# Kernel optimization log

Measured on AMD Instinct MI355X. Metric: run time of the kernel, lower is better.

## Reference

```python
import math
import jax, jax.numpy as jnp
import numpy as np

B, T, D = 2, 2048, 2048
NH, HD = 16, 48           # query heads, head dim
LAT, NLH = 256, 8         # latent dim, latent (kv) heads
EPS = 1e-5


def setup_inputs() -> dict:
    key = jax.random.key(0)
    ks = jax.random.split(key, 7)
    x = jax.random.normal(ks[0], (B, T, D), dtype=jnp.float32)
    # causal mask [B, 1, T, T]
    mask = jnp.broadcast_to(jnp.tril(jnp.ones((T, T), dtype=bool))[None, None], (B, 1, T, T))
    s = lambda fan_in: 1.0 / math.sqrt(fan_in)
    Wq = jax.random.normal(ks[1], (D, NH * HD), dtype=jnp.float32) * s(D)
    Wkv = jax.random.normal(ks[2], (D, LAT), dtype=jnp.float32) * s(D)
    w_norm = jnp.ones((LAT,), dtype=jnp.float32)
    Wk = jax.random.normal(ks[3], (LAT, NLH * HD), dtype=jnp.float32) * s(LAT)
    Wv = jax.random.normal(ks[4], (LAT, NLH * HD), dtype=jnp.float32) * s(LAT)
    Wo = jax.random.normal(ks[5], (NH * HD, D), dtype=jnp.float32) * s(NH * HD)
    return {"x": x, "mask": mask, "Wq": Wq, "Wkv": Wkv, "w_norm": w_norm,
            "Wk": Wk, "Wv": Wv, "Wo": Wo}


def rms_norm(x, weight, eps=EPS):
    var = jnp.mean(x * x, axis=-1, keepdims=True)
    return x * jax.lax.rsqrt(var + eps) * weight


def reference(x, mask, Wq, Wkv, w_norm, Wk, Wv, Wo):
    b, t, _ = x.shape
    q = (x @ Wq).reshape(b, t, NH, HD)                      # [B,T,NH,HD]
    kv_latent = rms_norm(x @ Wkv, w_norm)                   # [B,T,LAT]
    k = (kv_latent @ Wk).reshape(b, t, NLH, HD)             # [B,T,NLH,HD]
    v = (kv_latent @ Wv).reshape(b, t, NLH, HD)
    rep = NH // NLH
    k = jnp.repeat(k, rep, axis=2)                          # [B,T,NH,HD]
    v = jnp.repeat(v, rep, axis=2)
    q = q.transpose(0, 2, 1, 3)                             # [B,NH,T,HD]
    k = k.transpose(0, 2, 1, 3)
    v = v.transpose(0, 2, 1, 3)
    scale = 1.0 / math.sqrt(HD)
    scores = jnp.einsum('bhqd,bhkd->bhqk', q, k) * scale    # [B,NH,T,T]
    scores = jnp.where(mask, scores, -1e9)
    attn = jax.nn.softmax(scores, axis=-1)
    out = jnp.einsum('bhqk,bhkd->bhqd', attn, v)            # [B,NH,T,HD]
    out = out.transpose(0, 2, 1, 3).reshape(b, t, NH * HD)
    return out @ Wo                                          # [B,T,D]
```

## Files before the change

kernel.cpp:

```cpp
#include <hip/hip_runtime.h>
#include <hip/hip_bf16.h>

typedef __hip_bfloat16 bf16;
typedef __attribute__((ext_vector_type(8))) short short8;
typedef __attribute__((ext_vector_type(4))) float f32x4;

#define Bq   2
#define Tq   2048
#define Dq   2048
#define NHq  16
#define HDq  48
#define LATq 256
#define NLHq 8
#define QN   (NHq * HDq)
#define KVN  (NLHq * HDq)

__device__ __forceinline__ unsigned short f2u(float x) {
    __hip_bfloat16 h = __float2bfloat16(x);
    return *reinterpret_cast<unsigned short*>(&h);
}
__device__ __forceinline__ float u2f(unsigned short u) {
    return __uint_as_float((unsigned)u << 16);
}
__device__ __forceinline__ unsigned pk2(float a, float b) {
    return (unsigned)f2u(a) | ((unsigned)f2u(b) << 16);
}

__global__ void __launch_bounds__(256)
cvt_x(const float* __restrict__ in, bf16* __restrict__ out) {
    const size_t i = ((size_t)blockIdx.x * 256 + threadIdx.x) * 8;
    const float4 a = *(const float4*)&in[i];
    const float4 b = *(const float4*)&in[i + 4];
    uint4 u;
    u.x = pk2(a.x, a.y); u.y = pk2(a.z, a.w);
    u.z = pk2(b.x, b.y); u.w = pk2(b.z, b.w);
    *(uint4*)&out[i] = u;
}

__global__ void __launch_bounds__(256)
tr_w(const float* __restrict__ W, bf16* __restrict__ WT, int K, int N) {
    __shared__ float ts[32][33];
    const int n0 = blockIdx.x * 32, k0 = blockIdx.y * 32;
    const int t = threadIdx.x;
    const int r = t >> 3, c4 = (t & 7) * 4;
    const float4 v = *(const float4*)&W[(size_t)(k0 + r) * N + n0 + c4];
    ts[r][c4] = v.x; ts[r][c4 + 1] = v.y; ts[r][c4 + 2] = v.z; ts[r][c4 + 3] = v.w;
    __syncthreads();
    const unsigned u0 = pk2(ts[c4][r], ts[c4 + 1][r]);
    const unsigned u1 = pk2(ts[c4 + 2][r], ts[c4 + 3][r]);
    *(uint2*)&WT[(size_t)(n0 + r) * K + k0 + c4] = make_uint2(u0, u1);
}

template<int MODE>
__global__ void __launch_bounds__(512)
gemm128(const bf16* __restrict__ A, const bf16* __restrict__ BT,
        void* __restrict__ C0v, void* __restrict__ C1v, int K) {
    __shared__ short As[2][128 * 40];
    __shared__ short Bs[2][64 * 40];
    const int t  = threadIdx.x;
    const int m0 = blockIdx.x * 128;
    const int n0 = blockIdx.y * 64;
    const int w  = t >> 6;
    const int wm = (w & 3) * 32;
    const int wn = (w >> 2) * 32;
    const int lr = t & 15;
    const int quad = (t >> 4) & 3;
    const int sr = t >> 2, sc = t & 3;

    f32x4 acc[2][2];
    #pragma unroll
    for (int mi = 0; mi < 2; ++mi)
        #pragma unroll
        for (int ni = 0; ni < 2; ++ni) acc[mi][ni] = (f32x4){0.f, 0.f, 0.f, 0.f};

    int aoff[2], boff[2];
    #pragma unroll
    for (int mi = 0; mi < 2; ++mi) aoff[mi] = (wm + mi * 16 + lr) * 40 + quad * 8;
    #pragma unroll
    for (int ni = 0; ni < 2; ++ni) boff[ni] = (wn + ni * 16 + lr) * 40 + quad * 8;

    uint4 pa0, pb0;
    auto glo = [&](int kt) {
        const int kb = kt * 32 + sc * 8;
        pa0 = *(const uint4*)&A[(size_t)(m0 + sr) * K + kb];
        if (t < 256) pb0 = *(const uint4*)&BT[(size_t)(n0 + sr) * K + kb];
    };
    auto lwrite = [&](int bb) {
        *(uint4*)&As[bb][sr * 40 + sc * 8] = pa0;
        if (t < 256) *(uint4*)&Bs[bb][sr * 40 + sc * 8] = pb0;
    };

    const int nk = K / 32;
    glo(0);
    lwrite(0);
    glo(1);
    __syncthreads();
    int cur = 0;

    for (int kt = 0; kt < nk; ++kt) {
        short8 af[2], bfr[2];
        #pragma unroll
        for (int mi = 0; mi < 2; ++mi) af[mi] = *(const short8*)&As[cur][aoff[mi]];
        #pragma unroll
        for (int ni = 0; ni < 2; ++ni) bfr[ni] = *(const short8*)&Bs[cur][boff[ni]];
        #pragma unroll
        for (int mi = 0; mi < 2; ++mi)
            #pragma unroll
            for (int ni = 0; ni < 2; ++ni)
                acc[mi][ni] = __builtin_amdgcn_mfma_f32_16x16x32_bf16(af[mi], bfr[ni], acc[mi][ni], 0, 0, 0);
        if (kt + 1 < nk) lwrite(cur ^ 1);
        if (kt + 2 < nk) glo(kt + 2);
        __syncthreads();
        cur ^= 1;
    }

    #pragma unroll
    for (int mi = 0; mi < 2; ++mi)
        #pragma unroll
        for (int ni = 0; ni < 2; ++ni) {
            const int col = n0 + wn + ni * 16 + lr;
            #pragma unroll
            for (int r = 0; r < 4; ++r) {
                const int row = m0 + wm + mi * 16 + quad * 4 + r;
                const float v = acc[mi][ni][r];
                if constexpr (MODE == 0) {
                    if (col < QN) ((bf16*)C0v)[(size_t)row * QN + col] = __float2bfloat16(v);
                    else ((float*)C1v)[(size_t)row * LATq + (col - QN)] = v;
                } else if constexpr (MODE == 1) {
                    if (col < KVN) ((bf16*)C0v)[(size_t)row * KVN + col] = __float2bfloat16(v);
                    else ((bf16*)C1v)[(size_t)row * KVN + (col - KVN)] = __float2bfloat16(v);
                } else {
                    ((float*)C0v)[(size_t)row * Dq + col] = v;
                }
            }
        }
}

__global__ void __launch_bounds__(256)
mla_kvrms(const float* __restrict__ xkv, const float* __restrict__ wn,
          bf16* __restrict__ lat) {
    const int t = threadIdx.x;
    const int row = blockIdx.x * 4 + (t >> 6);
    const int lane = t & 63;
    const float4 v = *(const float4*)&xkv[(size_t)row * LATq + lane * 4];
    float ss = v.x * v.x + v.y * v.y + v.z * v.z + v.w * v.w;
    ss += __shfl_xor(ss, 1);  ss += __shfl_xor(ss, 2);  ss += __shfl_xor(ss, 4);
    ss += __shfl_xor(ss, 8);  ss += __shfl_xor(ss, 16); ss += __shfl_xor(ss, 32);
    const float rr = rsqrtf(ss * (1.0f / LATq) + 1e-5f);
    const float4 g = *(const float4*)&wn[lane * 4];
    const unsigned w0 = pk2(v.x * rr * g.x, v.y * rr * g.y);
    const unsigned w1 = pk2(v.z * rr * g.z, v.w * rr * g.w);
    *(uint2*)&lat[(size_t)row * LATq + lane * 4] = make_uint2(w0, w1);
}

__global__ void __launch_bounds__(512)
mla_attn(const bf16* __restrict__ q, const bf16* __restrict__ kk,
         const bf16* __restrict__ vv, bf16* __restrict__ ao) {
    __shared__ __align__(16) short Ks[2][64 * 48];
    __shared__ __align__(16) short Vt[2][48 * 72];
    __shared__ __align__(16) short Ps[8][16 * 72];
    const int t    = threadIdx.x;
    const int g    = blockIdx.x;
    const int qy   = blockIdx.y;
    const int b    = blockIdx.z;
    const int qt0  = (qy < 16) ? (qy << 1) : (63 - (qy << 1));
    const int qt   = b ? (31 - qt0) : qt0;
    const int w    = t >> 6;
    const int lane = t & 63;
    const int lr   = t & 15;
    const int quad = (t >> 4) & 3;
    const int hh   = w & 1;
    const int rh   = w >> 1;
    const int h    = g * 2 + hh;
    const float scale = 0.14433756729740643f;
    const short8 z8 = {0, 0, 0, 0, 0, 0, 0, 0};

    const int qloc = rh * 16 + lr;
    const int qg   = qt * 64 + qloc;
    const bf16* qr = q + (size_t)(b * Tq + qg) * QN + h * HDq;
    short8 qf0 = *(const short8*)(qr + quad * 8);
    const short8 q1 = *(const short8*)(qr + 32 + (quad & 1) * 8);
    short8 qf1 = (quad < 2) ? q1 : z8;

    const bf16* kb = kk + (size_t)b * Tq * KVN + g * HDq;
    const bf16* vb = vv + (size_t)b * Tq * KVN + g * HDq;

    float m = -1e30f, l = 0.f;
    f32x4 acc[3];
    #pragma unroll
    for (int dm = 0; dm < 3; ++dm) acc[dm] = (f32x4){0.f, 0.f, 0.f, 0.f};

    short* Pw = &Ps[w][0];
    uint4 pre[3];

    auto issue = [&](int tl) {
        if (w >= 4) return;
        #pragma unroll
        for (int r = 0; r < 3; ++r) {
            if (w < 2) {
                const int idx = (w * 3 + r) * 64 + lane;
                const int row = idx / 6, ch = idx - row * 6;
                pre[r] = *(const uint4*)(kb + (size_t)(tl * 64 + row) * KVN + ch * 8);
            } else {
                const int idx = ((w - 2) * 3 + r) * 64 + lane;
                const int kp = idx & 31, hc = idx >> 5;
                const bf16* src = vb + (size_t)(tl * 64 + 2 * kp) * KVN + hc * 4;
                const uint2 a2 = *(const uint2*)src;
                const uint2 b2 = *(const uint2*)(src + KVN);
                pre[r].x = a2.x; pre[r].y = a2.y; pre[r].z = b2.x; pre[r].w = b2.y;
            }
        }
    };
    auto lwrite = [&](int bb) {
        if (w >= 4) return;
        #pragma unroll
        for (int r = 0; r < 3; ++r) {
            if (w < 2) {
                const int idx = (w * 3 + r) * 64 + lane;
                const int row = idx / 6, ch = idx - row * 6;
                *(uint4*)&Ks[bb][row * 48 + ch * 8] = pre[r];
            } else {
                const int idx = ((w - 2) * 3 + r) * 64 + lane;
                const int kp = idx & 31, hc = idx >> 5;
                const unsigned short* uu = (const unsigned short*)&pre[r];
                #pragma unroll
                for (int j = 0; j < 4; ++j)
                    *(unsigned*)&Vt[bb][(hc * 4 + j) * 72 + 2 * kp] =
                        (unsigned)uu[j] | ((unsigned)uu[4 + j] << 16);
            }
        }
    };

    issue(0);
    lwrite(0);
    __syncthreads();
    int cur = 0;

    for (int tl = 0; tl <= qt; ++tl) {
        const bool pref = (tl < qt);
        if (pref) issue(tl + 1);

        f32x4 sc[4];
        #pragma unroll
        for (int mt = 0; mt < 4; ++mt) {
            const short8 k0 = *(const short8*)&Ks[cur][(mt * 16 + lr) * 48 + quad * 8];
            const short8 k1v = *(const short8*)&Ks[cur][(mt * 16 + lr) * 48 + 32 + (quad & 1) * 8];
            const short8 k1 = (quad < 2) ? k1v : z8;
            f32x4 s = (f32x4){0.f, 0.f, 0.f, 0.f};
            s = __builtin_amdgcn_mfma_f32_16x16x32_bf16(k0, qf0, s, 0, 0, 0);
            s = __builtin_amdgcn_mfma_f32_16x16x32_bf16(k1, qf1, s, 0, 0, 0);
            sc[mt] = s;
        }
        if (tl == qt) {
            #pragma unroll
            for (int mt = 0; mt < 4; ++mt)
                #pragma unroll
                for (int r = 0; r < 4; ++r)
                    if (mt * 16 + quad * 4 + r > qloc) sc[mt][r] = -1e30f;
        }
        float mx = -1e30f;
        #pragma unroll
        for (int mt = 0; mt < 4; ++mt)
            #pragma unroll
            for (int r = 0; r < 4; ++r) mx = fmaxf(mx, sc[mt][r]);
        mx = fmaxf(mx, __shfl_xor(mx, 16));
        mx = fmaxf(mx, __shfl_xor(mx, 32));
        const float mn = fmaxf(m, mx * scale);
        const float f  = __expf(m - mn);
        m = mn;
        float rs = 0.f;
        #pragma unroll
        for (int mt = 0; mt < 4; ++mt)
            #pragma unroll
            for (int r = 0; r < 4; ++r) {
                const float p = u2f(f2u(__expf(fmaf(sc[mt][r], scale, -mn))));
                sc[mt][r] = p;
                rs += p;
            }
        rs += __shfl_xor(rs, 16);
        rs += __shfl_xor(rs, 32);
        l = l * f + rs;
        #pragma unroll
        for (int dm = 0; dm < 3; ++dm)
            #pragma unroll
            for (int r = 0; r < 4; ++r) acc[dm][r] *= f;
        #pragma unroll
        for (int mt = 0; mt < 4; ++mt) {
            unsigned* pw = (unsigned*)&Pw[lr * 72 + mt * 16 + quad * 4];
            pw[0] = pk2(sc[mt][0], sc[mt][1]);
            pw[1] = pk2(sc[mt][2], sc[mt][3]);
        }
        const short8 pf0 = *(const short8*)&Pw[lr * 72 + quad * 8];
        const short8 pf1 = *(const short8*)&Pw[lr * 72 + 32 + quad * 8];
        #pragma unroll
        for (int dm = 0; dm < 3; ++dm) {
            const short8 v0 = *(const short8*)&Vt[cur][(dm * 16 + lr) * 72 + quad * 8];
            const short8 v1 = *(const short8*)&Vt[cur][(dm * 16 + lr) * 72 + 32 + quad * 8];
            acc[dm] = __builtin_amdgcn_mfma_f32_16x16x32_bf16(v0, pf0, acc[dm], 0, 0, 0);
            acc[dm] = __builtin_amdgcn_mfma_f32_16x16x32_bf16(v1, pf1, acc[dm], 0, 0, 0);
        }

        if (pref) lwrite(cur ^ 1);
        __syncthreads();
        cur ^= 1;
    }

    const float inv = 1.0f / l;
    bf16* orow = ao + (size_t)(b * Tq + qg) * QN + h * HDq;
    #pragma unroll
    for (int dm = 0; dm < 3; ++dm) {
        const unsigned w0 = pk2(acc[dm][0] * inv, acc[dm][1] * inv);
        const unsigned w1 = pk2(acc[dm][2] * inv, acc[dm][3] * inv);
        *(uint2*)(orow + dm * 16 + quad * 4) = make_uint2(w0, w1);
    }
}

extern "C" void kernel_launch(void* const* d_in, const int* in_sizes, int n_in,
                              void* d_out, int out_size, void* d_ws, size_t ws_size,
                              hipStream_t stream) {
    const float* x   = (const float*)d_in[0];
    const float* Wq  = (const float*)d_in[2];
    const float* Wkv = (const float*)d_in[3];
    const float* wn  = (const float*)d_in[4];
    const float* Wk  = (const float*)d_in[5];
    const float* Wv  = (const float*)d_in[6];
    const float* Wo  = (const float*)d_in[7];
    float* out = (float*)d_out;

    const int M = Bq * Tq;
    char* ob = (char*)d_out;
    bf16*  xb    = (bf16*)ob;
    bf16*  qws   = (bf16*)(ob + 16777216);
    float* xkv   = (float*)(ob + 23068672);
    bf16*  latb  = (bf16*)(ob + 27262976);
    bf16*  WqkvT = (bf16*)(ob + 29360128);
    bf16*  WkvpT = (bf16*)ob;
    bf16*  kws = (bf16*)d_ws;
    bf16*  vws = kws + (size_t)M * KVN;
    bf16*  aob = vws + (size_t)M * KVN;
    bf16*  WoT = (bf16*)d_ws;

    cvt_x <<<4096, 256, 0, stream>>>(x, xb);
    tr_w  <<<dim3(QN / 32, Dq / 32), 256, 0, stream>>>(Wq, WqkvT, Dq, QN);
    tr_w  <<<dim3(LATq / 32, Dq / 32), 256, 0, stream>>>(Wkv, WqkvT + (size_t)QN * Dq, Dq, LATq);
    gemm128<0> <<<dim3(M / 128, 1024 / 64), 512, 0, stream>>>(xb, WqkvT, qws, xkv, Dq);
    tr_w  <<<dim3(KVN / 32, LATq / 32), 256, 0, stream>>>(Wk, WkvpT, LATq, KVN);
    tr_w  <<<dim3(KVN / 32, LATq / 32), 256, 0, stream>>>(Wv, WkvpT + (size_t)KVN * LATq, LATq, KVN);
    mla_kvrms <<<M / 4, 256, 0, stream>>>(xkv, wn, latb);
    gemm128<1> <<<dim3(M / 128, 768 / 64), 512, 0, stream>>>(latb, WkvpT, kws, vws, LATq);
    mla_attn <<<dim3(NLHq, 32, Bq), 512, 0, stream>>>(qws, kws, vws, aob);
    tr_w  <<<dim3(Dq / 32, QN / 32), 256, 0, stream>>>(Wo, WoT, QN, Dq);
    gemm128<2> <<<dim3(M / 128, Dq / 64), 512, 0, stream>>>(aob, WoT, out, nullptr, QN);
}
```

Before: 262.8 us.

## Merge prep kernels into combined launches and use separate staging registers in GEMM loop

Folds the x conversion and the Wq/Wkv transposes into one kernel, and the RMS norm plus the Wk/Wv transposes into a second, cutting the number of launches. The GEMM main loop is unrolled by two with alternating prefetch register sets, and __syncthreads is replaced by a barrier that waits only on LDS counters, so global loads can stay in flight across the barrier. Workspace aliasing is also changed: xkv now lives in the attention-output buffer and WoT in the k workspace. The risk is the weaker barrier, which depends on global loads not being needed before the LDS write that follows.

```diff
diff --git a/kernel.cpp b/kernel.cpp
--- a/kernel.cpp
+++ b/kernel.cpp
@@ -26,22 +26,16 @@
     return (unsigned)f2u(a) | ((unsigned)f2u(b) << 16);
 }
 
-__global__ void __launch_bounds__(256)
-cvt_x(const float* __restrict__ in, bf16* __restrict__ out) {
-    const size_t i = ((size_t)blockIdx.x * 256 + threadIdx.x) * 8;
-    const float4 a = *(const float4*)&in[i];
-    const float4 b = *(const float4*)&in[i + 4];
-    uint4 u;
-    u.x = pk2(a.x, a.y); u.y = pk2(a.z, a.w);
-    u.z = pk2(b.x, b.y); u.w = pk2(b.z, b.w);
-    *(uint4*)&out[i] = u;
-}
-
-__global__ void __launch_bounds__(256)
-tr_w(const float* __restrict__ W, bf16* __restrict__ WT, int K, int N) {
+__device__ __forceinline__ void lds_barrier() {
+    asm volatile("s_waitcnt lgkmcnt(0)" ::: "memory");
+    __builtin_amdgcn_s_barrier();
+    asm volatile("" ::: "memory");
+}
+
+__device__ __forceinline__ void tr_tile(const float* __restrict__ W,
+                                        bf16* __restrict__ WT,
+                                        int K, int N, int n0, int k0, int t) {
     __shared__ float ts[32][33];
-    const int n0 = blockIdx.x * 32, k0 = blockIdx.y * 32;
-    const int t = threadIdx.x;
     const int r = t >> 3, c4 = (t & 7) * 4;
     const float4 v = *(const float4*)&W[(size_t)(k0 + r) * N + n0 + c4];
     ts[r][c4] = v.x; ts[r][c4 + 1] = v.y; ts[r][c4 + 2] = v.z; ts[r][c4 + 3] = v.w;
@@ -49,6 +43,61 @@
     const unsigned u0 = pk2(ts[c4][r], ts[c4 + 1][r]);
     const unsigned u1 = pk2(ts[c4 + 2][r], ts[c4 + 3][r]);
     *(uint2*)&WT[(size_t)(n0 + r) * K + k0 + c4] = make_uint2(u0, u1);
+}
+
+__global__ void __launch_bounds__(256)
+tr_w(const float* __restrict__ W, bf16* __restrict__ WT, int K, int N) {
+    tr_tile(W, WT, K, N, blockIdx.x * 32, blockIdx.y * 32, threadIdx.x);
+}
+
+__global__ void __launch_bounds__(256)
+prep1(const float* __restrict__ x, const float* __restrict__ Wq,
+      const float* __restrict__ Wkv, bf16* __restrict__ xb,
+      bf16* __restrict__ WqkvT) {
+    const int bid = blockIdx.x;
+    const int t = threadIdx.x;
+    if (bid < 4096) {
+        const size_t i = ((size_t)bid * 256 + t) * 8;
+        const float4 a = *(const float4*)&x[i];
+        const float4 b = *(const float4*)&x[i + 4];
+        uint4 u;
+        u.x = pk2(a.x, a.y); u.y = pk2(a.z, a.w);
+        u.z = pk2(b.x, b.y); u.w = pk2(b.z, b.w);
+        *(uint4*)&xb[i] = u;
+    } else if (bid < 5632) {
+        const int l = bid - 4096;
+        tr_tile(Wq, WqkvT, Dq, QN, (l % 24) * 32, (l / 24) * 32, t);
+    } else {
+        const int l = bid - 5632;
+        tr_tile(Wkv, WqkvT + (size_t)QN * Dq, Dq, LATq, (l % 8) * 32, (l / 8) * 32, t);
+    }
+}
+
+__global__ void __launch_bounds__(256)
+prep2(const float* __restrict__ xkv, const float* __restrict__ wn,
+      const float* __restrict__ Wk, const float* __restrict__ Wv,
+      bf16* __restrict__ lat, bf16* __restrict__ WkvpT) {
+    const int bid = blockIdx.x;
+    const int t = threadIdx.x;
+    if (bid < 1024) {
+        const int row = bid * 4 + (t >> 6);
+        const int lane = t & 63;
+        const float4 v = *(const float4*)&xkv[(size_t)row * LATq + lane * 4];
+        float ss = v.x * v.x + v.y * v.y + v.z * v.z + v.w * v.w;
+        ss += __shfl_xor(ss, 1);  ss += __shfl_xor(ss, 2);  ss += __shfl_xor(ss, 4);
+        ss += __shfl_xor(ss, 8);  ss += __shfl_xor(ss, 16); ss += __shfl_xor(ss, 32);
+        const float rr = rsqrtf(ss * (1.0f / LATq) + 1e-5f);
+        const float4 g = *(const float4*)&wn[lane * 4];
+        const unsigned w0 = pk2(v.x * rr * g.x, v.y * rr * g.y);
+        const unsigned w1 = pk2(v.z * rr * g.z, v.w * rr * g.w);
+        *(uint2*)&lat[(size_t)row * LATq + lane * 4] = make_uint2(w0, w1);
+    } else if (bid < 1120) {
+        const int l = bid - 1024;
+        tr_tile(Wk, WkvpT, LATq, KVN, (l % 12) * 32, (l / 12) * 32, t);
+    } else {
+        const int l = bid - 1120;
+        tr_tile(Wv, WkvpT + (size_t)KVN * LATq, LATq, KVN, (l % 12) * 32, (l / 12) * 32, t);
+    }
 }
 
 template<int MODE>
@@ -79,38 +128,56 @@
     #pragma unroll
     for (int ni = 0; ni < 2; ++ni) boff[ni] = (wn + ni * 16 + lr) * 40 + quad * 8;
 
-    uint4 pa0, pb0;
-    auto glo = [&](int kt) {
+    uint4 a0, b0, a1, b1;
+    auto glo0 = [&](int kt) {
         const int kb = kt * 32 + sc * 8;
-        pa0 = *(const uint4*)&A[(size_t)(m0 + sr) * K + kb];
-        if (t < 256) pb0 = *(const uint4*)&BT[(size_t)(n0 + sr) * K + kb];
-    };
-    auto lwrite = [&](int bb) {
-        *(uint4*)&As[bb][sr * 40 + sc * 8] = pa0;
-        if (t < 256) *(uint4*)&Bs[bb][sr * 40 + sc * 8] = pb0;
-    };
-
-    const int nk = K / 32;
-    glo(0);
-    lwrite(0);
-    glo(1);
-    __syncthreads();
-    int cur = 0;
-
-    for (int kt = 0; kt < nk; ++kt) {
+        a0 = *(const uint4*)&A[(size_t)(m0 + sr) * K + kb];
+        if (t < 256) b0 = *(const uint4*)&BT[(size_t)(n0 + sr) * K + kb];
+    };
+    auto glo1 = [&](int kt) {
+        const int kb = kt * 32 + sc * 8;
+        a1 = *(const uint4*)&A[(size_t)(m0 + sr) * K + kb];
+        if (t < 256) b1 = *(const uint4*)&BT[(size_t)(n0 + sr) * K + kb];
+    };
+    auto lw0 = [&](int bb) {
+        *(uint4*)&As[bb][sr * 40 + sc * 8] = a0;
+        if (t < 256) *(uint4*)&Bs[bb][sr * 40 + sc * 8] = b0;
+    };
+    auto lw1 = [&](int bb) {
+        *(uint4*)&As[bb][sr * 40 + sc * 8] = a1;
+        if (t < 256) *(uint4*)&Bs[bb][sr * 40 + sc * 8] = b1;
+    };
+    auto compute = [&](int bb) {
         short8 af[2], bfr[2];
         #pragma unroll
-        for (int mi = 0; mi < 2; ++mi) af[mi] = *(const short8*)&As[cur][aoff[mi]];
-        #pragma unroll
-        for (int ni = 0; ni < 2; ++ni) bfr[ni] = *(const short8*)&Bs[cur][boff[ni]];
+        for (int mi = 0; mi < 2; ++mi) af[mi] = *(const short8*)&As[bb][aoff[mi]];
+        #pragma unroll
+        for (int ni = 0; ni < 2; ++ni) bfr[ni] = *(const short8*)&Bs[bb][boff[ni]];
         #pragma unroll
         for (int mi = 0; mi < 2; ++mi)
             #pragma unroll
             for (int ni = 0; ni < 2; ++ni)
                 acc[mi][ni] = __builtin_amdgcn_mfma_f32_16x16x32_bf16(af[mi], bfr[ni], acc[mi][ni], 0, 0, 0);
-        if (kt + 1 < nk) lwrite(cur ^ 1);
-        if (kt + 2 < nk) glo(kt + 2);
-        __syncthreads();
+    };
+
+    const int nk = K / 32;
+    glo0(0);
+    lw0(0);
+    glo1(1);
+    lds_barrier();
+    int cur = 0;
+
+    for (int kt = 0; kt < nk; kt += 2) {
+        compute(cur);
+        if (kt + 2 < nk) glo0(kt + 2);
+        lw1(cur ^ 1);
+        lds_barrier();
+        cur ^= 1;
+
+        compute(cur);
+        if (kt + 3 < nk) glo1(kt + 3);
+        if (kt + 2 < nk) lw0(cur ^ 1);
+        lds_barrier();
         cur ^= 1;
     }
 
@@ -134,23 +201,6 @@
                 }
             }
         }
-}
-
-__global__ void __launch_bounds__(256)
-mla_kvrms(const float* __restrict__ xkv, const float* __restrict__ wn,
-          bf16* __restrict__ lat) {
-    const int t = threadIdx.x;
-    const int row = blockIdx.x * 4 + (t >> 6);
-    const int lane = t & 63;
-    const float4 v = *(const float4*)&xkv[(size_t)row * LATq + lane * 4];
-    float ss = v.x * v.x + v.y * v.y + v.z * v.z + v.w * v.w;
-    ss += __shfl_xor(ss, 1);  ss += __shfl_xor(ss, 2);  ss += __shfl_xor(ss, 4);
-    ss += __shfl_xor(ss, 8);  ss += __shfl_xor(ss, 16); ss += __shfl_xor(ss, 32);
-    const float rr = rsqrtf(ss * (1.0f / LATq) + 1e-5f);
-    const float4 g = *(const float4*)&wn[lane * 4];
-    const unsigned w0 = pk2(v.x * rr * g.x, v.y * rr * g.y);
-    const unsigned w1 = pk2(v.z * rr * g.z, v.w * rr * g.w);
-    *(uint2*)&lat[(size_t)row * LATq + lane * 4] = make_uint2(w0, w1);
 }
 
 __global__ void __launch_bounds__(512)
@@ -330,25 +380,21 @@
     const int M = Bq * Tq;
     char* ob = (char*)d_out;
     bf16*  xb    = (bf16*)ob;
+    bf16*  WkvpT = (bf16*)ob;
     bf16*  qws   = (bf16*)(ob + 16777216);
-    float* xkv   = (float*)(ob + 23068672);
     bf16*  latb  = (bf16*)(ob + 27262976);
     bf16*  WqkvT = (bf16*)(ob + 29360128);
-    bf16*  WkvpT = (bf16*)ob;
     bf16*  kws = (bf16*)d_ws;
     bf16*  vws = kws + (size_t)M * KVN;
     bf16*  aob = vws + (size_t)M * KVN;
-    bf16*  WoT = (bf16*)d_ws;
-
-    cvt_x <<<4096, 256, 0, stream>>>(x, xb);
-    tr_w  <<<dim3(QN / 32, Dq / 32), 256, 0, stream>>>(Wq, WqkvT, Dq, QN);
-    tr_w  <<<dim3(LATq / 32, Dq / 32), 256, 0, stream>>>(Wkv, WqkvT + (size_t)QN * Dq, Dq, LATq);
+    float* xkv = (float*)aob;
+    bf16*  WoT = kws;
+
+    prep1 <<<6144, 256, 0, stream>>>(x, Wq, Wkv, xb, WqkvT);
     gemm128<0> <<<dim3(M / 128, 1024 / 64), 512, 0, stream>>>(xb, WqkvT, qws, xkv, Dq);
-    tr_w  <<<dim3(KVN / 32, LATq / 32), 256, 0, stream>>>(Wk, WkvpT, LATq, KVN);
-    tr_w  <<<dim3(KVN / 32, LATq / 32), 256, 0, stream>>>(Wv, WkvpT + (size_t)KVN * LATq, LATq, KVN);
-    mla_kvrms <<<M / 4, 256, 0, stream>>>(xkv, wn, latb);
+    prep2 <<<1216, 256, 0, stream>>>(xkv, wn, Wk, Wv, latb, WkvpT);
     gemm128<1> <<<dim3(M / 128, 768 / 64), 512, 0, stream>>>(latb, WkvpT, kws, vws, LATq);
     mla_attn <<<dim3(NLHq, 32, Bq), 512, 0, stream>>>(qws, kws, vws, aob);
-    tr_w  <<<dim3(Dq / 32, QN / 32), 256, 0, stream>>>(Wo, WoT, QN, Dq);
+    tr_w <<<dim3(Dq / 32, QN / 32), 256, 0, stream>>>(Wo, WoT, QN, Dq);
     gemm128<2> <<<dim3(M / 128, Dq / 64), 512, 0, stream>>>(aob, WoT, out, nullptr, QN);
 }
```

Measured after the change: 258.6 us. About the same (-1.6%).
